# Kernel optimization log

Measured on AMD Instinct MI355X. Metric: run time of the kernel, lower is better.

Reference implementation:

```python
import jax, jax.numpy as jnp
import numpy as np

E = 16          # expert_num
T = 8192        # token_num
H = 1024        # hidden_size
I = 4096        # intermediate_size
LN_EPS = 1e-12


def setup_inputs() -> dict:
    key = jax.random.key(0)
    ks = jax.random.split(key, 6)
    hidden_states = jax.random.normal(ks[0], (T, H), dtype=jnp.float32)
    perm = jax.random.permutation(ks[1], T).astype(jnp.int32)
    s1 = 1.0 / np.sqrt(H)
    s2 = 1.0 / np.sqrt(I)
    w1 = jax.random.uniform(ks[2], (E, I, H), jnp.float32, -s1, s1)
    b1 = jax.random.uniform(ks[3], (E, I), jnp.float32, -s1, s1)
    w2 = jax.random.uniform(ks[4], (E, H, I), jnp.float32, -s2, s2)
    b2 = jax.random.uniform(ks[5], (E, H), jnp.float32, -s2, s2)
    ln_gamma = jnp.ones((H,), jnp.float32)
    ln_beta = jnp.zeros((H,), jnp.float32)
    return {"hidden_states": hidden_states, "perm": perm, "w1": w1, "b1": b1,
            "w2": w2, "b2": b2, "ln_gamma": ln_gamma, "ln_beta": ln_beta}


def _layer_norm(x, gamma, beta, eps):
    mu = jnp.mean(x, axis=-1, keepdims=True)
    var = jnp.var(x, axis=-1, keepdims=True)
    return (x - mu) * jax.lax.rsqrt(var + eps) * gamma + beta


def reference(hidden_states, perm, w1, b1, w2, b2, ln_gamma, ln_beta):
    # dispatch: gather tokens by random permutation, group per expert
    xp = hidden_states[perm].reshape(E, T // E, H)            # [E, T/E, H]
    # grouped expert FFN (batched GEMM replaces the per-expert Python loop)
    h = jnp.einsum('eth,eih->eti', xp, w1) + b1[:, None, :]   # [E, T/E, I]
    h = jax.nn.gelu(h, approximate=False)
    o = jnp.einsum('eti,ehi->eth', h, w2) + b2[:, None, :]    # [E, T/E, H]
    # scatter-restore via inverse permutation
    restore = jnp.argsort(perm)
    o = o.reshape(T, H)[restore]
    # dropout is identity (p=0, eval); residual + LayerNorm
    return _layer_norm(o + hidden_states, ln_gamma, ln_beta, LN_EPS)
```

## Files before the change

kernel.cpp:

```cpp
#include <hip/hip_runtime.h>
#include <hip/hip_bf16.h>
#include <stdint.h>

#define E_NUM 16
#define T_NUM 8192
#define H_DIM 1024
#define I_DIM 4096
#define MPE   512

typedef __attribute__((ext_vector_type(8))) short short8;
typedef __attribute__((ext_vector_type(4))) float f32x4;
using bf16 = __hip_bfloat16;

typedef const __attribute__((address_space(1))) void GLV;
typedef __attribute__((address_space(3))) void LDSV;

__device__ __forceinline__ uint32_t pack2_bf16(float a, float b) {
  union { float f; uint32_t u; } ua, ub;
  ua.f = a; ub.f = b;
  uint32_t x = ua.u + (0x7FFFu + ((ua.u >> 16) & 1u));
  uint32_t y = ub.u + (0x7FFFu + ((ub.u >> 16) & 1u));
  return (x >> 16) | (y & 0xFFFF0000u);
}

__device__ __forceinline__ short8 cvt8(f32x4 a, f32x4 b) {
  union { short8 s; __hip_bfloat162 h[4]; } r;
  r.h[0] = __float22bfloat162_rn({a[0], a[1]});
  r.h[1] = __float22bfloat162_rn({a[2], a[3]});
  r.h[2] = __float22bfloat162_rn({b[0], b[1]});
  r.h[3] = __float22bfloat162_rn({b[2], b[3]});
  return r.s;
}

__global__ __launch_bounds__(256)
void gather_cast_kernel(const float* __restrict__ hs, const int* __restrict__ perm,
                        uint32_t* __restrict__ xp) {
  const int r = blockIdx.x;
  const int t = threadIdx.x;
  const int src = perm[r];
  float4 v = ((const float4*)(hs + (size_t)src * H_DIM))[t];
  uint2 o;
  o.x = pack2_bf16(v.x, v.y);
  o.y = pack2_bf16(v.z, v.w);
  ((uint2*)(xp + (size_t)r * (H_DIM / 2)))[t] = o;
}

template<int EPI, int KSPLIT, int N, int KFULL, int KLEN, int LOG_NBN>
__global__ __launch_bounds__(1024, 4)
void moe_gemm_kernel(const bf16* __restrict__ A, const float* __restrict__ Bw,
                     const float* __restrict__ bias, bf16* __restrict__ Hout,
                     float* __restrict__ Pout) {
  constexpr int NK = KLEN / 32;
  __shared__ bf16  As[2][512 * 32];
  __shared__ float Bs[2][128 * 32];

  const int nwg = gridDim.x, qx = nwg >> 3, orig = blockIdx.x;
  const int wg = (orig & 7) * qx + (orig >> 3);
  const int bn   = wg & ((1 << LOG_NBN) - 1);
  const int rest = wg >> LOG_NBN;
  const int ks = (KSPLIT == 2) ? (rest & 1) : 0;
  const int e  = (KSPLIT == 2) ? (rest >> 1) : rest;
  const int K0 = ks * KLEN;

  const int tid = threadIdx.x;
  const int l = tid & 63;
  const int w = tid >> 6;
  const int wr = w >> 1, wc = w & 1;
  const int fr = l & 15, fq = l >> 4;
  const int rx = fr & 7;

  const bf16*  Ae = A  + (size_t)e * MPE * KFULL + K0;
  const float* Be = Bw + ((size_t)e * N + (size_t)bn * 128) * KFULL + K0;

  const int apq = tid >> 3;
  const int ag  = (tid & 7) ^ (apq & 7);
  const bf16* Asrc0 = Ae + (size_t)(apq       + 256 * (ag >> 2)) * KFULL + (ag & 3) * 8;
  const bf16* Asrc1 = Ae + (size_t)(apq + 128 + 256 * (ag >> 2)) * KFULL + (ag & 3) * 8;

  const float* Bsrc = Be + (size_t)(tid >> 3) * KFULL + ((tid & 7) ^ ((tid >> 3) & 7)) * 4;

  const int aso = (((((wr >> 2) << 2)) | fq) ^ rx) * 8;
  const int bp0 = (((fq << 1))     ^ rx) * 4;
  const int bp1 = (((fq << 1) | 1) ^ rx) * 4;

#define STAGE(buf, kt)                                                              \
  {                                                                                 \
    __builtin_amdgcn_global_load_lds((GLV*)(Asrc0 + (kt) * 32),                     \
                                     (LDSV*)&As[buf][tid * 8], 16, 0, 0);           \
    __builtin_amdgcn_global_load_lds((GLV*)(Asrc1 + (kt) * 32),                     \
                                     (LDSV*)&As[buf][(1024 + tid) * 8], 16, 0, 0);  \
    __builtin_amdgcn_global_load_lds((GLV*)(Bsrc + (kt) * 32),                      \
                                     (LDSV*)&Bs[buf][tid * 4], 16, 0, 0);           \
  }

  f32x4 acc[4][4];
#pragma unroll
  for (int m = 0; m < 4; ++m)
#pragma unroll
    for (int n = 0; n < 4; ++n) acc[m][n] = (f32x4){0.f, 0.f, 0.f, 0.f};

  STAGE(0, 0);
  __syncthreads();

  for (int t = 0; t < NK; ++t) {
    const int cur = t & 1, nxt = cur ^ 1;
    if (t + 1 < NK) STAGE(nxt, t + 1);

    short8 a8[4];
#pragma unroll
    for (int m = 0; m < 4; ++m)
      a8[m] = *(const short8*)&As[cur][((wr & 3) * 64 + m * 16 + fr) * 64 + aso];

#pragma unroll
    for (int n = 0; n < 4; ++n) {
      const int col = wc * 64 + n * 16 + fr;
      const f32x4 x0 = *(const f32x4*)&Bs[cur][col * 32 + bp0];
      const f32x4 x1 = *(const f32x4*)&Bs[cur][col * 32 + bp1];
      const short8 b8 = cvt8(x0, x1);
#pragma unroll
      for (int m = 0; m < 4; ++m)
        acc[m][n] = __builtin_amdgcn_mfma_f32_16x16x32_bf16(a8[m], b8, acc[m][n], 0, 0, 0);
    }

    __syncthreads();
  }
#undef STAGE

  if (EPI == 1) {
    float bv[4];
#pragma unroll
    for (int n = 0; n < 4; ++n)
      bv[n] = bias[(size_t)e * N + bn * 128 + wc * 64 + n * 16 + fr];
    bf16* He = Hout + (size_t)e * MPE * N;
#pragma unroll
    for (int m = 0; m < 4; ++m) {
#pragma unroll
      for (int j = 0; j < 4; ++j) {
        const int row = wr * 64 + m * 16 + fq * 4 + j;
#pragma unroll
        for (int n = 0; n < 4; ++n) {
          const int col = bn * 128 + wc * 64 + n * 16 + fr;
          float x = acc[m][n][j] + bv[n];
          float g = 0.5f * x * (1.0f + erff(x * 0.70710678118654752f));
          He[(size_t)row * N + col] = __float2bfloat16(g);
        }
      }
    }
  } else {
    float* Pd = Pout + (size_t)ks * T_NUM * H_DIM + (size_t)e * MPE * N;
#pragma unroll
    for (int m = 0; m < 4; ++m) {
#pragma unroll
      for (int j = 0; j < 4; ++j) {
        const int row = wr * 64 + m * 16 + fq * 4 + j;
#pragma unroll
        for (int n = 0; n < 4; ++n) {
          const int col = bn * 128 + wc * 64 + n * 16 + fr;
          Pd[(size_t)row * N + col] = acc[m][n][j];
        }
      }
    }
  }
}

__global__ __launch_bounds__(256)
void ln_resid2_kernel(float* __restrict__ out, const float* __restrict__ hs,
                      const float* __restrict__ p0, const float* __restrict__ p1,
                      const float* __restrict__ b2, const float* __restrict__ gamma,
                      const float* __restrict__ beta, const int* __restrict__ perm,
                      const int two) {
  const int r = blockIdx.x;
  const int t = threadIdx.x;
  const int e = r >> 9;
  const int drow = perm[r];
  float4 a = ((const float4*)(p0 + (size_t)r * H_DIM))[t];
  if (two) {
    float4 b = ((const float4*)(p1 + (size_t)r * H_DIM))[t];
    a.x += b.x; a.y += b.y; a.z += b.z; a.w += b.w;
  }
  float4 bb = ((const float4*)(b2 + (size_t)e * H_DIM))[t];
  float4 h  = ((const float4*)(hs + (size_t)drow * H_DIM))[t];
  float v0 = a.x + bb.x + h.x, v1 = a.y + bb.y + h.y;
  float v2 = a.z + bb.z + h.z, v3 = a.w + bb.w + h.w;
  float s  = v0 + v1 + v2 + v3;
  float sq = v0 * v0 + v1 * v1 + v2 * v2 + v3 * v3;
#pragma unroll
  for (int off = 32; off > 0; off >>= 1) {
    s  += __shfl_down(s, off);
    sq += __shfl_down(sq, off);
  }
  __shared__ float ss[4], ssq[4];
  const int wv = t >> 6;
  if ((t & 63) == 0) { ss[wv] = s; ssq[wv] = sq; }
  __syncthreads();
  s  = ss[0] + ss[1] + ss[2] + ss[3];
  sq = ssq[0] + ssq[1] + ssq[2] + ssq[3];
  const float mu  = s * (1.0f / (float)H_DIM);
  const float var = sq * (1.0f / (float)H_DIM) - mu * mu;
  const float rs  = rsqrtf(var + 1e-12f);
  float4 g = ((const float4*)gamma)[t];
  float4 b = ((const float4*)beta)[t];
  float4 rr;
  rr.x = (v0 - mu) * rs * g.x + b.x;
  rr.y = (v1 - mu) * rs * g.y + b.y;
  rr.z = (v2 - mu) * rs * g.z + b.z;
  rr.w = (v3 - mu) * rs * g.w + b.w;
  ((float4*)(out + (size_t)drow * H_DIM))[t] = rr;
}

extern "C" void kernel_launch(void* const* d_in, const int* in_sizes, int n_in,
                              void* d_out, int out_size, void* d_ws, size_t ws_size,
                              hipStream_t stream) {
  const float* hs    = (const float*)d_in[0];
  const int*   perm  = (const int*)d_in[1];
  const float* w1    = (const float*)d_in[2];
  const float* b1    = (const float*)d_in[3];
  const float* w2    = (const float*)d_in[4];
  const float* b2    = (const float*)d_in[5];
  const float* gamma = (const float*)d_in[6];
  const float* beta  = (const float*)d_in[7];
  float* out = (float*)d_out;

  const size_t xp_b   = (size_t)T_NUM * H_DIM * sizeof(bf16);
  const size_t hbuf_b = (size_t)T_NUM * I_DIM * sizeof(bf16);
  const size_t part_b = (size_t)T_NUM * H_DIM * sizeof(float);

  bf16*  xp   = (bf16*)d_ws;
  bf16*  hbuf = (bf16*)((char*)d_ws + xp_b);
  float* pbuf = (float*)((char*)d_ws + xp_b + hbuf_b);

  gather_cast_kernel<<<T_NUM, 256, 0, stream>>>(hs, perm, (uint32_t*)xp);

  moe_gemm_kernel<1, 1, I_DIM, H_DIM, H_DIM, 5>
      <<<512, 1024, 0, stream>>>(xp, w1, b1, hbuf, nullptr);

  if (ws_size >= xp_b + hbuf_b + 2 * part_b) {
    moe_gemm_kernel<0, 2, H_DIM, I_DIM, I_DIM / 2, 3>
        <<<256, 1024, 0, stream>>>(hbuf, w2, nullptr, nullptr, pbuf);
    ln_resid2_kernel<<<T_NUM, 256, 0, stream>>>(out, hs, pbuf, pbuf + (size_t)T_NUM * H_DIM,
                                                b2, gamma, beta, perm, 1);
  } else {
    moe_gemm_kernel<0, 1, H_DIM, I_DIM, I_DIM, 3>
        <<<128, 1024, 0, stream>>>(hbuf, w2, nullptr, nullptr, pbuf);
    ln_resid2_kernel<<<T_NUM, 256, 0, stream>>>(out, hs, pbuf, nullptr,
                                                b2, gamma, beta, perm, 0);
  }
}
```

Baseline: 328.5 us.

## Split first GEMM into dedicated kernel with narrower N tile and fast GELU

The first expert GEMM gets its own kernel that uses a 64-wide N tile instead of 128, launching 1024 workgroups instead of 512 and halving the accumulator registers per thread. Its launch bound changes from 4 to 2 blocks per multiprocessor. The exact erf GELU is replaced by a tanh-style approximation built from exp and a hardware reciprocal, which cuts transcendental cost in the epilogue but slightly changes numerics. The second GEMM is kept as before with the unused epilogue branch removed. The narrower tile means the activation tile is reloaded for twice as many workgroups, raising A-side traffic.

Result: slower. 344.4 us (+4.8%).

```diff
diff --git a/kernel.cpp b/kernel.cpp
--- a/kernel.cpp
+++ b/kernel.cpp
@@ -30,6 +30,11 @@
   r.h[2] = __float22bfloat162_rn({b[0], b[1]});
   r.h[3] = __float22bfloat162_rn({b[2], b[3]});
   return r.s;
+}
+
+__device__ __forceinline__ float fast_gelu(float x) {
+  const float p = x * fmaf(x * x, -0.0713548162726f, -1.59576912161f);
+  return x * __builtin_amdgcn_rcpf(1.0f + __expf(p));
 }
 
 __global__ __launch_bounds__(256)
@@ -45,11 +50,112 @@
   ((uint2*)(xp + (size_t)r * (H_DIM / 2)))[t] = o;
 }
 
-template<int EPI, int KSPLIT, int N, int KFULL, int KLEN, int LOG_NBN>
+template<int LOG_NBN, int NWG>
+__global__ __launch_bounds__(1024, 2)
+void moe_gemm1_kernel(const bf16* __restrict__ A, const float* __restrict__ Bw,
+                      const float* __restrict__ bias, bf16* __restrict__ Hout) {
+  constexpr int N = I_DIM, K = H_DIM;
+  constexpr int NK = K / 32;
+  __shared__ bf16  As[2][512 * 32];
+  __shared__ float Bs[2][64 * 32];
+
+  constexpr int qx = NWG >> 3;
+  const int orig = blockIdx.x;
+  const int wg = (orig & 7) * qx + (orig >> 3);
+  const int bn = wg & ((1 << LOG_NBN) - 1);
+  const int e  = wg >> LOG_NBN;
+
+  const int tid = threadIdx.x;
+  const int l = tid & 63;
+  const int w = tid >> 6;
+  const int wr = w >> 1, wc = w & 1;
+  const int fr = l & 15, fq = l >> 4;
+  const int rx = fr & 7;
+
+  const bf16*  Ae = A  + (size_t)e * MPE * K;
+  const float* Be = Bw + ((size_t)e * N + (size_t)bn * 64) * K;
+
+  const int apq = tid >> 3;
+  const int ag  = (tid & 7) ^ (apq & 7);
+  const bf16* As0 = Ae + (size_t)(apq       + 256 * (ag >> 2)) * K + (ag & 3) * 8;
+  const bf16* As1 = Ae + (size_t)(apq + 128 + 256 * (ag >> 2)) * K + (ag & 3) * 8;
+
+  const int brow = tid >> 3;
+  const float* Bsrc = Be + (size_t)(brow & 63) * K + ((tid & 7) ^ (brow & 7)) * 4;
+
+#define STAGE1(buf, kt)                                                            \
+  {                                                                                \
+    __builtin_amdgcn_global_load_lds((GLV*)(As0 + (kt) * 32),                      \
+        (LDSV*)((char*)&As[buf][0] + tid * 16), 16, 0, 0);                         \
+    __builtin_amdgcn_global_load_lds((GLV*)(As1 + (kt) * 32),                      \
+        (LDSV*)((char*)&As[buf][0] + 16384 + tid * 16), 16, 0, 0);                 \
+    if (tid < 512)                                                                 \
+      __builtin_amdgcn_global_load_lds((GLV*)(Bsrc + (kt) * 32),                   \
+          (LDSV*)((char*)&Bs[buf][0] + tid * 16), 16, 0, 0);                       \
+  }
+
+  const int aoff  = ((wr & 3) * 64 + fr) * 128 + ((((wr >> 2) << 2) | fq) ^ rx) * 16;
+  const int b0off = (wc * 32 + fr) * 128 + (((fq << 1)) ^ rx) * 16;
+  const int b1off = (wc * 32 + fr) * 128 + (((fq << 1) | 1) ^ rx) * 16;
+
+  f32x4 acc[4][2];
+#pragma unroll
+  for (int m = 0; m < 4; ++m)
+#pragma unroll
+    for (int n = 0; n < 2; ++n) acc[m][n] = (f32x4){0.f, 0.f, 0.f, 0.f};
+
+  STAGE1(0, 0);
+  __syncthreads();
+
+  for (int t = 0; t < NK; ++t) {
+    const int cur = t & 1;
+    if (t + 1 < NK) STAGE1(cur ^ 1, t + 1);
+
+    short8 a8[4];
+#pragma unroll
+    for (int m = 0; m < 4; ++m)
+      a8[m] = *(const short8*)((const char*)&As[cur][0] + aoff + m * 2048);
+    short8 b8[2];
+#pragma unroll
+    for (int n = 0; n < 2; ++n) {
+      const f32x4 x0 = *(const f32x4*)((const char*)&Bs[cur][0] + b0off + n * 2048);
+      const f32x4 x1 = *(const f32x4*)((const char*)&Bs[cur][0] + b1off + n * 2048);
+      b8[n] = cvt8(x0, x1);
+    }
+#pragma unroll
+    for (int m = 0; m < 4; ++m)
+#pragma unroll
+      for (int n = 0; n < 2; ++n)
+        acc[m][n] = __builtin_amdgcn_mfma_f32_16x16x32_bf16(a8[m], b8[n], acc[m][n], 0, 0, 0);
+
+    __syncthreads();
+  }
+#undef STAGE1
+
+  float bv[2];
+#pragma unroll
+  for (int n = 0; n < 2; ++n)
+    bv[n] = bias[(size_t)e * N + bn * 64 + wc * 32 + n * 16 + fr];
+
+  bf16* He = Hout + (size_t)e * MPE * N;
+#pragma unroll
+  for (int m = 0; m < 4; ++m) {
+#pragma unroll
+    for (int j = 0; j < 4; ++j) {
+      const int row = wr * 64 + m * 16 + fq * 4 + j;
+#pragma unroll
+      for (int n = 0; n < 2; ++n) {
+        const int col = bn * 64 + wc * 32 + n * 16 + fr;
+        He[(size_t)row * N + col] = __float2bfloat16(fast_gelu(acc[m][n][j] + bv[n]));
+      }
+    }
+  }
+}
+
+template<int KSPLIT, int N, int KFULL, int KLEN, int LOG_NBN>
 __global__ __launch_bounds__(1024, 4)
-void moe_gemm_kernel(const bf16* __restrict__ A, const float* __restrict__ Bw,
-                     const float* __restrict__ bias, bf16* __restrict__ Hout,
-                     float* __restrict__ Pout) {
+void moe_gemm2_kernel(const bf16* __restrict__ A, const float* __restrict__ Bw,
+                      float* __restrict__ Pout) {
   constexpr int NK = KLEN / 32;
   __shared__ bf16  As[2][512 * 32];
   __shared__ float Bs[2][128 * 32];
@@ -74,20 +180,19 @@
 
   const int apq = tid >> 3;
   const int ag  = (tid & 7) ^ (apq & 7);
-  const bf16* Asrc0 = Ae + (size_t)(apq       + 256 * (ag >> 2)) * KFULL + (ag & 3) * 8;
-  const bf16* Asrc1 = Ae + (size_t)(apq + 128 + 256 * (ag >> 2)) * KFULL + (ag & 3) * 8;
-
+  const bf16* As0 = Ae + (size_t)(apq       + 256 * (ag >> 2)) * KFULL + (ag & 3) * 8;
+  const bf16* As1 = Ae + (size_t)(apq + 128 + 256 * (ag >> 2)) * KFULL + (ag & 3) * 8;
   const float* Bsrc = Be + (size_t)(tid >> 3) * KFULL + ((tid & 7) ^ ((tid >> 3) & 7)) * 4;
 
   const int aso = (((((wr >> 2) << 2)) | fq) ^ rx) * 8;
   const int bp0 = (((fq << 1))     ^ rx) * 4;
   const int bp1 = (((fq << 1) | 1) ^ rx) * 4;
 
-#define STAGE(buf, kt)                                                              \
+#define STAGE2(buf, kt)                                                             \
   {                                                                                 \
-    __builtin_amdgcn_global_load_lds((GLV*)(Asrc0 + (kt) * 32),                     \
+    __builtin_amdgcn_global_load_lds((GLV*)(As0 + (kt) * 32),                       \
                                      (LDSV*)&As[buf][tid * 8], 16, 0, 0);           \
-    __builtin_amdgcn_global_load_lds((GLV*)(Asrc1 + (kt) * 32),                     \
+    __builtin_amdgcn_global_load_lds((GLV*)(As1 + (kt) * 32),                       \
                                      (LDSV*)&As[buf][(1024 + tid) * 8], 16, 0, 0);  \
     __builtin_amdgcn_global_load_lds((GLV*)(Bsrc + (kt) * 32),                      \
                                      (LDSV*)&Bs[buf][tid * 4], 16, 0, 0);           \
@@ -99,18 +204,17 @@
 #pragma unroll
     for (int n = 0; n < 4; ++n) acc[m][n] = (f32x4){0.f, 0.f, 0.f, 0.f};
 
-  STAGE(0, 0);
+  STAGE2(0, 0);
   __syncthreads();
 
   for (int t = 0; t < NK; ++t) {
-    const int cur = t & 1, nxt = cur ^ 1;
-    if (t + 1 < NK) STAGE(nxt, t + 1);
+    const int cur = t & 1;
+    if (t + 1 < NK) STAGE2(cur ^ 1, t + 1);
 
     short8 a8[4];
 #pragma unroll
     for (int m = 0; m < 4; ++m)
       a8[m] = *(const short8*)&As[cur][((wr & 3) * 64 + m * 16 + fr) * 64 + aso];
-
 #pragma unroll
     for (int n = 0; n < 4; ++n) {
       const int col = wc * 64 + n * 16 + fr;
@@ -121,43 +225,20 @@
       for (int m = 0; m < 4; ++m)
         acc[m][n] = __builtin_amdgcn_mfma_f32_16x16x32_bf16(a8[m], b8, acc[m][n], 0, 0, 0);
     }
-
     __syncthreads();
   }
-#undef STAGE
-
-  if (EPI == 1) {
-    float bv[4];
-#pragma unroll
-    for (int n = 0; n < 4; ++n)
-      bv[n] = bias[(size_t)e * N + bn * 128 + wc * 64 + n * 16 + fr];
-    bf16* He = Hout + (size_t)e * MPE * N;
-#pragma unroll
-    for (int m = 0; m < 4; ++m) {
-#pragma unroll
-      for (int j = 0; j < 4; ++j) {
-        const int row = wr * 64 + m * 16 + fq * 4 + j;
-#pragma unroll
-        for (int n = 0; n < 4; ++n) {
-          const int col = bn * 128 + wc * 64 + n * 16 + fr;
-          float x = acc[m][n][j] + bv[n];
-          float g = 0.5f * x * (1.0f + erff(x * 0.70710678118654752f));
-          He[(size_t)row * N + col] = __float2bfloat16(g);
-        }
-      }
-    }
-  } else {
-    float* Pd = Pout + (size_t)ks * T_NUM * H_DIM + (size_t)e * MPE * N;
-#pragma unroll
-    for (int m = 0; m < 4; ++m) {
-#pragma unroll
-      for (int j = 0; j < 4; ++j) {
-        const int row = wr * 64 + m * 16 + fq * 4 + j;
-#pragma unroll
-        for (int n = 0; n < 4; ++n) {
-          const int col = bn * 128 + wc * 64 + n * 16 + fr;
-          Pd[(size_t)row * N + col] = acc[m][n][j];
-        }
+#undef STAGE2
+
+  float* Pd = Pout + (size_t)ks * T_NUM * H_DIM + (size_t)e * MPE * N;
+#pragma unroll
+  for (int m = 0; m < 4; ++m) {
+#pragma unroll
+    for (int j = 0; j < 4; ++j) {
+      const int row = wr * 64 + m * 16 + fq * 4 + j;
+#pragma unroll
+      for (int n = 0; n < 4; ++n) {
+        const int col = bn * 128 + wc * 64 + n * 16 + fr;
+        Pd[(size_t)row * N + col] = acc[m][n][j];
       }
     }
   }
@@ -231,17 +312,16 @@
 
   gather_cast_kernel<<<T_NUM, 256, 0, stream>>>(hs, perm, (uint32_t*)xp);
 
-  moe_gemm_kernel<1, 1, I_DIM, H_DIM, H_DIM, 5>
-      <<<512, 1024, 0, stream>>>(xp, w1, b1, hbuf, nullptr);
+  moe_gemm1_kernel<6, 1024><<<1024, 1024, 0, stream>>>(xp, w1, b1, hbuf);
 
   if (ws_size >= xp_b + hbuf_b + 2 * part_b) {
-    moe_gemm_kernel<0, 2, H_DIM, I_DIM, I_DIM / 2, 3>
-        <<<256, 1024, 0, stream>>>(hbuf, w2, nullptr, nullptr, pbuf);
+    moe_gemm2_kernel<2, H_DIM, I_DIM, I_DIM / 2, 3>
+        <<<256, 1024, 0, stream>>>(hbuf, w2, pbuf);
     ln_resid2_kernel<<<T_NUM, 256, 0, stream>>>(out, hs, pbuf, pbuf + (size_t)T_NUM * H_DIM,
                                                 b2, gamma, beta, perm, 1);
   } else {
-    moe_gemm_kernel<0, 1, H_DIM, I_DIM, I_DIM, 3>
-        <<<128, 1024, 0, stream>>>(hbuf, w2, nullptr, nullptr, pbuf);
+    moe_gemm2_kernel<1, H_DIM, I_DIM, I_DIM, 3>
+        <<<128, 1024, 0, stream>>>(hbuf, w2, pbuf);
     ln_resid2_kernel<<<T_NUM, 256, 0, stream>>>(out, hs, pbuf, nullptr,
                                                 b2, gamma, beta, perm, 0);
   }
```

## Use tanh-form GELU and stage GEMM1 epilogue through swizzled LDS for wide stores

Applied to the files above, without the earlier changes.

The GEMM1 epilogue now replaces the exact erf GELU with a sigmoid/exp tanh approximation using a hardware reciprocal. It also writes the bf16 results into the A-tile LDS buffer with an XOR swizzle, two halves of 256 rows at a time, then stores them to global memory as coalesced 16-byte vectors. Before, each lane wrote scattered 2-byte values. The cost is extra barriers, LDS traffic, and a small accuracy change from the approximate GELU.

Result: no change. 323.7 us (-1.5%).

```diff
diff --git a/kernel.cpp b/kernel.cpp
--- a/kernel.cpp
+++ b/kernel.cpp
@@ -30,6 +30,11 @@
   r.h[2] = __float22bfloat162_rn({b[0], b[1]});
   r.h[3] = __float22bfloat162_rn({b[2], b[3]});
   return r.s;
+}
+
+__device__ __forceinline__ float fast_gelu(float x) {
+  const float p = x * fmaf(x * x, -0.0713548162726f, -1.59576912161f);
+  return x * __builtin_amdgcn_rcpf(1.0f + __expf(p));
 }
 
 __global__ __launch_bounds__(256)
@@ -74,8 +79,8 @@
 
   const int apq = tid >> 3;
   const int ag  = (tid & 7) ^ (apq & 7);
-  const bf16* Asrc0 = Ae + (size_t)(apq       + 256 * (ag >> 2)) * KFULL + (ag & 3) * 8;
-  const bf16* Asrc1 = Ae + (size_t)(apq + 128 + 256 * (ag >> 2)) * KFULL + (ag & 3) * 8;
+  const bf16* As0 = Ae + (size_t)(apq       + 256 * (ag >> 2)) * KFULL + (ag & 3) * 8;
+  const bf16* As1 = Ae + (size_t)(apq + 128 + 256 * (ag >> 2)) * KFULL + (ag & 3) * 8;
 
   const float* Bsrc = Be + (size_t)(tid >> 3) * KFULL + ((tid & 7) ^ ((tid >> 3) & 7)) * 4;
 
@@ -85,9 +90,9 @@
 
 #define STAGE(buf, kt)                                                              \
   {                                                                                 \
-    __builtin_amdgcn_global_load_lds((GLV*)(Asrc0 + (kt) * 32),                     \
+    __builtin_amdgcn_global_load_lds((GLV*)(As0 + (kt) * 32),                       \
                                      (LDSV*)&As[buf][tid * 8], 16, 0, 0);           \
-    __builtin_amdgcn_global_load_lds((GLV*)(Asrc1 + (kt) * 32),                     \
+    __builtin_amdgcn_global_load_lds((GLV*)(As1 + (kt) * 32),                       \
                                      (LDSV*)&As[buf][(1024 + tid) * 8], 16, 0, 0);  \
     __builtin_amdgcn_global_load_lds((GLV*)(Bsrc + (kt) * 32),                      \
                                      (LDSV*)&Bs[buf][tid * 4], 16, 0, 0);           \
@@ -132,19 +137,37 @@
     for (int n = 0; n < 4; ++n)
       bv[n] = bias[(size_t)e * N + bn * 128 + wc * 64 + n * 16 + fr];
     bf16* He = Hout + (size_t)e * MPE * N;
-#pragma unroll
-    for (int m = 0; m < 4; ++m) {
-#pragma unroll
-      for (int j = 0; j < 4; ++j) {
-        const int row = wr * 64 + m * 16 + fq * 4 + j;
-#pragma unroll
-        for (int n = 0; n < 4; ++n) {
-          const int col = bn * 128 + wc * 64 + n * 16 + fr;
-          float x = acc[m][n][j] + bv[n];
-          float g = 0.5f * x * (1.0f + erff(x * 0.70710678118654752f));
-          He[(size_t)row * N + col] = __float2bfloat16(g);
+
+    bf16* Ls = &As[0][0];
+#pragma unroll
+    for (int P = 0; P < 2; ++P) {
+      if ((wr >> 2) == P) {
+        const int wrl = wr & 3;
+#pragma unroll
+        for (int m = 0; m < 4; ++m) {
+#pragma unroll
+          for (int j = 0; j < 4; ++j) {
+            const int lr = wrl * 64 + m * 16 + fq * 4 + j;
+#pragma unroll
+            for (int n = 0; n < 4; ++n) {
+              const int c = wc * 64 + n * 16 + fr;
+              const int byteoff = lr * 256 + ((c * 2) ^ ((lr & 7) << 4));
+              Ls[byteoff >> 1] = __float2bfloat16(fast_gelu(acc[m][n][j] + bv[n]));
+            }
+          }
         }
       }
+      __syncthreads();
+#pragma unroll
+      for (int q = 0; q < 4; ++q) {
+        const int o = (tid + q * 1024) * 16;
+        const int lr = o >> 8;
+        const int cb = o & 255;
+        const int sb = lr * 256 + (cb ^ ((lr & 7) << 4));
+        uint4 v = *(const uint4*)((const char*)Ls + sb);
+        *(uint4*)&He[(size_t)(P * 256 + lr) * N + bn * 128 + (cb >> 1)] = v;
+      }
+      __syncthreads();
     }
   } else {
     float* Pd = Pout + (size_t)ks * T_NUM * H_DIM + (size_t)e * MPE * N;
```
